# Optimization experiments

Measured on AMD Instinct MI355X. Metric: run time of the kernel, lower is better.

Reference implementation:

```python
import jax, jax.numpy as jnp
import numpy as np

N_NODES = 50000
N_EDGES = 800000
IN_FEATS = 256
H_FEATS = 256
NUM_CLASSES = 128


def setup_inputs() -> dict:
    key = jax.random.key(0)
    ks = jax.random.split(key, 5)
    x = jax.random.normal(ks[0], (N_NODES, IN_FEATS), dtype=jnp.float32)
    src = jax.random.randint(ks[1], (N_EDGES,), 0, N_NODES, dtype=jnp.int64)
    dst = jax.random.randint(ks[2], (N_EDGES,), 0, N_NODES, dtype=jnp.int64)
    W1 = jax.random.normal(ks[3], (IN_FEATS, H_FEATS), dtype=jnp.float32) * (1.0 / np.sqrt(IN_FEATS))
    b1 = jnp.zeros((H_FEATS,), dtype=jnp.float32)
    W2 = jax.random.normal(ks[4], (H_FEATS, NUM_CLASSES), dtype=jnp.float32) * (1.0 / np.sqrt(H_FEATS))
    b2 = jnp.zeros((NUM_CLASSES,), dtype=jnp.float32)
    return {"x": x, "src": src, "dst": dst, "W1": W1, "b1": b1, "W2": W2, "b2": b2}


def _graph_conv(x, src, dst, norm_src, norm_dst, W, b):
    # DGL GraphConv, norm='both': D_out^{-1/2} A D_in^{-1/2} X W + b
    # project first (in_feats >= out_feats -> cheaper messages), math identical
    h = (x * norm_src[:, None]) @ W                      # [N, out]
    agg = jax.ops.segment_sum(h[src], dst, num_segments=N_NODES)  # gather + scatter-add
    return agg * norm_dst[:, None] + b


def reference(x, src, dst, W1, b1, W2, b2):
    ones = jnp.ones((N_EDGES,), dtype=x.dtype)
    deg_out = jax.ops.segment_sum(ones, src, num_segments=N_NODES)
    deg_in = jax.ops.segment_sum(ones, dst, num_segments=N_NODES)
    norm_src = jnp.clip(deg_out, 1.0, None) ** -0.5
    norm_dst = jnp.clip(deg_in, 1.0, None) ** -0.5

    h = _graph_conv(x, src, dst, norm_src, norm_dst, W1, b1)
    h = jax.nn.relu(h)
    out = _graph_conv(h, src, dst, norm_src, norm_dst, W2, b2)
    return out
```

## Files before the change

kernel.cpp:

```cpp
#include <hip/hip_runtime.h>

#define NNODES 50000
#define MPAD   50048
#define NEDGES 800000
#define KDIM   256
#define FH     256
#define FOUT   128
#define FCH    32

#define SHIFT  8
#define NBUCK  196
#define NB1    200
#define EPB    4000

typedef __bf16 bf16x8 __attribute__((ext_vector_type(8)));
typedef float floatx4 __attribute__((ext_vector_type(4)));
typedef float floatx2 __attribute__((ext_vector_type(2)));

struct int4u { int x, y, z, w; };

__device__ __forceinline__ float bf2f(unsigned short u) {
    union { unsigned int i; float f; } v;
    v.i = ((unsigned int)u) << 16;
    return v.f;
}
__device__ __forceinline__ unsigned short f2bf(float f) {
    union { float f; unsigned int i; } v;
    v.f = f;
    unsigned int r = v.i + 0x7FFFu + ((v.i >> 16) & 1u);
    return (unsigned short)(r >> 16);
}

__device__ __forceinline__ void acc_pairs(floatx2* acc, uint4 v) {
    unsigned int d[4] = {v.x, v.y, v.z, v.w};
#pragma unroll
    for (int k = 0; k < 4; ++k) {
        union { unsigned int u; float f; } lo, hi;
        lo.u = d[k] << 16;
        hi.u = d[k] & 0xFFFF0000u;
        floatx2 p = {lo.f, hi.f};
        acc[k] += p;
    }
}

__global__ __launch_bounds__(256) void l1_sort_cast(const int* __restrict__ src,
                                                    const int* __restrict__ dst,
                                                    unsigned int* __restrict__ tmp1,
                                                    unsigned char* __restrict__ tmp2,
                                                    int* __restrict__ exD_arr,
                                                    int* __restrict__ exS_arr,
                                                    const float* __restrict__ W1,
                                                    unsigned short* __restrict__ Wt1,
                                                    const float* __restrict__ W2,
                                                    unsigned short* __restrict__ Wt2) {
    __shared__ int histD[256], histS[256], exD[256], exS[256];
    __shared__ unsigned int bufD[EPB];
    __shared__ unsigned short bufS[EPB];
    __shared__ float tile[32][33];
    const int tid = threadIdx.x;

    if (blockIdx.x >= NB1) {
        int b = blockIdx.x - NB1;
        const float* W; unsigned short* Wt; int N;
        if (b < 64) { W = W1; Wt = Wt1; N = FH; }
        else        { b -= 64; W = W2; Wt = Wt2; N = FOUT; }
        int kt = (b & 7) * 32;
        int nt = (b >> 3) * 32;
        int tx = tid & 31;
        int ty = tid >> 5;
        for (int r = ty; r < 32; r += 8)
            tile[r][tx] = W[(size_t)(kt + r) * N + nt + tx];
        __syncthreads();
        for (int r = ty; r < 32; r += 8)
            Wt[(size_t)(nt + r) * KDIM + kt + tx] = f2bf(tile[tx][r]);
        return;
    }

    const int b = blockIdx.x;
    const int base = b * EPB;
    histD[tid] = 0; histS[tid] = 0;
    __syncthreads();
    for (int g = tid; g < EPB / 4; g += 256) {
        uint4 s4 = *(const uint4*)(src + base + g * 4);
        uint4 d4 = *(const uint4*)(dst + base + g * 4);
        atomicAdd(&histD[d4.x >> SHIFT], 1);
        atomicAdd(&histD[d4.y >> SHIFT], 1);
        atomicAdd(&histD[d4.z >> SHIFT], 1);
        atomicAdd(&histD[d4.w >> SHIFT], 1);
        atomicAdd(&histS[s4.x >> SHIFT], 1);
        atomicAdd(&histS[s4.y >> SHIFT], 1);
        atomicAdd(&histS[s4.z >> SHIFT], 1);
        atomicAdd(&histS[s4.w >> SHIFT], 1);
    }
    __syncthreads();
    int vD = histD[tid], vS = histS[tid];
    exD[tid] = vD; exS[tid] = vS;
    __syncthreads();
    for (int off = 1; off < 256; off <<= 1) {
        int tD = (tid >= off) ? exD[tid - off] : 0;
        int tS = (tid >= off) ? exS[tid - off] : 0;
        __syncthreads();
        exD[tid] += tD; exS[tid] += tS;
        __syncthreads();
    }
    int eD = exD[tid] - vD, eS = exS[tid] - vS;
    exD_arr[tid * NB1 + b] = eD;
    exS_arr[tid * NB1 + b] = eS;
    __syncthreads();
    histD[tid] = eD; histS[tid] = eS;
    __syncthreads();
    for (int g = tid; g < EPB / 4; g += 256) {
        uint4 s4 = *(const uint4*)(src + base + g * 4);
        uint4 d4 = *(const uint4*)(dst + base + g * 4);
        unsigned int ss[4] = {s4.x, s4.y, s4.z, s4.w};
        unsigned int dd[4] = {d4.x, d4.y, d4.z, d4.w};
#pragma unroll
        for (int j = 0; j < 4; ++j) {
            int p = atomicAdd(&histD[dd[j] >> SHIFT], 1);
            bufD[p] = (ss[j] << 16) | dd[j];
            int q = atomicAdd(&histS[ss[j] >> SHIFT], 1);
            bufS[q] = (unsigned short)ss[j];
        }
    }
    __syncthreads();
    for (int e = tid; e < EPB; e += 256) tmp1[base + e] = bufD[e];
    for (int e = tid; e < EPB; e += 256) tmp2[base + e] = (unsigned char)(bufS[e] & 255u);
}

__global__ __launch_bounds__(256) void l2_both(const unsigned int* __restrict__ tmp1,
                                               const unsigned char* __restrict__ tmp2,
                                               const int* __restrict__ exD_arr,
                                               const int* __restrict__ exS_arr,
                                               int* __restrict__ row_ptr,
                                               float* __restrict__ norm_dst,
                                               float* __restrict__ norm_src,
                                               int* __restrict__ csr_src) {
    __shared__ int cnt[256], ofs[256], cur[256], red[256];
    __shared__ int segoff[NB1], seglen[NB1];
    const int tid = threadIdx.x;

    if (blockIdx.x >= NBUCK) {
        const int k = blockIdx.x - NBUCK;
        if (tid < NB1) {
            int e0 = exS_arr[k * NB1 + tid];
            segoff[tid] = tid * EPB + e0;
            seglen[tid] = exS_arr[(k + 1) * NB1 + tid] - e0;
        }
        cnt[tid] = 0;
        __syncthreads();
        if (tid < NB1) {
            int so = segoff[tid], sl = seglen[tid];
            for (int i = 0; i < sl; ++i)
                atomicAdd(&cnt[tmp2[so + i]], 1);
        }
        __syncthreads();
        int node = k * 256 + tid;
        if (node < NNODES) {
            int d = cnt[tid] < 1 ? 1 : cnt[tid];
            norm_src[node] = 1.0f / sqrtf((float)d);
        }
        return;
    }

    const int k = blockIdx.x;
    int e0v = 0;
    if (tid < NB1) {
        e0v = exD_arr[k * NB1 + tid];
        segoff[tid] = tid * EPB + e0v;
        seglen[tid] = exD_arr[(k + 1) * NB1 + tid] - e0v;
    }
    red[tid] = (tid < NB1) ? e0v : 0;
    cnt[tid] = 0;
    __syncthreads();
    for (int off = 128; off > 0; off >>= 1) {
        if (tid < off) red[tid] += red[tid + off];
        __syncthreads();
    }
    const int base = red[0];
    if (tid < NB1) {
        int so = segoff[tid], sl = seglen[tid];
        for (int i = 0; i < sl; ++i)
            atomicAdd(&cnt[tmp1[so + i] & 255u], 1);
    }
    __syncthreads();
    int v = cnt[tid];
    ofs[tid] = v;
    __syncthreads();
    for (int off = 1; off < 256; off <<= 1) {
        int t = (tid >= off) ? ofs[tid - off] : 0;
        __syncthreads();
        ofs[tid] += t;
        __syncthreads();
    }
    int excl = ofs[tid] - v;
    int node = k * 256 + tid;
    if (node < NNODES) {
        row_ptr[node] = base + excl;
        int d = v < 1 ? 1 : v;
        norm_dst[node] = 1.0f / sqrtf((float)d);
    }
    cur[tid] = base + excl;
    if (k == 0 && tid == 0) row_ptr[NNODES] = NEDGES;
    __syncthreads();
    if (tid < NB1) {
        int so = segoff[tid], sl = seglen[tid];
        for (int i = 0; i < sl; ++i) {
            unsigned int p = tmp1[so + i];
            int pos = atomicAdd(&cur[p & 255u], 1);
            csr_src[pos] = (int)(p >> 16);
        }
    }
}

struct arawF { float4 v[8]; float sc; };
struct arawU { uint4 v[4]; };
template <typename TA> struct rawsel;
template <> struct rawsel<float> { using type = arawF; };
template <> struct rawsel<unsigned short> { using type = arawU; };

__device__ __forceinline__ void loadA_raw(const float* A, const float* norm,
                                          int mt, int arow, int akseg, arawF& r) {
    int row = mt * 64 + arow;
    if (row < NNODES) {
        const float* p = A + (size_t)row * KDIM + akseg;
#pragma unroll
        for (int j = 0; j < 8; ++j) r.v[j] = *(const float4*)(p + j * 4);
        r.sc = norm[row];
    } else {
        float4 z = {0.f, 0.f, 0.f, 0.f};
#pragma unroll
        for (int j = 0; j < 8; ++j) r.v[j] = z;
        r.sc = 0.f;
    }
}
__device__ __forceinline__ void loadA_raw(const unsigned short* A, const float*,
                                          int mt, int arow, int akseg, arawU& r) {
    const unsigned short* p = A + ((size_t)(akseg >> 5) * MPAD + mt * 64 + arow) * FCH;
#pragma unroll
    for (int j = 0; j < 4; ++j) r.v[j] = *(const uint4*)(p + j * 8);
}
__device__ __forceinline__ void writeA_lds(char* Asb, int arow, int akseg, const arawF& r) {
    const int s = (arow & 7) << 4;
    const int base = arow * 512;
#pragma unroll
    for (int j = 0; j < 4; ++j) {
        union { uint4 u; unsigned short h[8]; } o;
        float4 a = r.v[2 * j], b = r.v[2 * j + 1];
        o.h[0] = f2bf(a.x * r.sc); o.h[1] = f2bf(a.y * r.sc);
        o.h[2] = f2bf(a.z * r.sc); o.h[3] = f2bf(a.w * r.sc);
        o.h[4] = f2bf(b.x * r.sc); o.h[5] = f2bf(b.y * r.sc);
        o.h[6] = f2bf(b.z * r.sc); o.h[7] = f2bf(b.w * r.sc);
        *(uint4*)(Asb + base + (((akseg + j * 8) * 2) ^ s)) = o.u;
    }
}
__device__ __forceinline__ void writeA_lds(char* Asb, int arow, int akseg, const arawU& r) {
    const int s = (arow & 7) << 4;
    const int base = arow * 512;
#pragma unroll
    for (int j = 0; j < 4; ++j)
        *(uint4*)(Asb + base + (((akseg + j * 8) * 2) ^ s)) = r.v[j];
}

template <typename TA, bool SCALE, int NPANEL>
__global__ __launch_bounds__(512) void gemm_bres(const TA* __restrict__ A,
                                                 const unsigned short* __restrict__ Bt,
                                                 const float* __restrict__ norm,
                                                 unsigned short* __restrict__ C) {
    constexpr int NTILES = MPAD / 64;
    __shared__ __align__(16) unsigned short Bs[128 * 256];
    __shared__ __align__(16) unsigned short As[64 * 256];
    char* Bsb = (char*)Bs;
    char* Asb = (char*)As;

    const int tid = threadIdx.x;
    const int lane = tid & 63;
    const int wave = tid >> 6;

    int col0, mt0, mstep;
    if (NPANEL == 2) {
        col0 = ((blockIdx.x >> 3) & 1) * 128;
        mt0 = ((blockIdx.x >> 4) << 3) + (blockIdx.x & 7);
        mstep = gridDim.x >> 1;
    } else {
        col0 = 0;
        mt0 = blockIdx.x;
        mstep = gridDim.x;
    }

    {
        int col = tid >> 2;
        int kq = (tid & 3) * 64;
        const unsigned short* bg = Bt + (size_t)(col0 + col) * KDIM + kq;
        const int s = (col & 7) << 4;
        const int base = col * 512;
#pragma unroll
        for (int j = 0; j < 8; ++j) {
            uint4 v = *(const uint4*)(bg + j * 8);
            *(uint4*)(Bsb + base + (((kq + j * 8) * 2) ^ s)) = v;
        }
    }

    const int arow = tid >> 3;
    const int akseg = (tid & 7) * 32;

    typename rawsel<TA>::type buf;
    loadA_raw(A, norm, mt0, arow, akseg, buf);
    writeA_lds(Asb, arow, akseg, buf);
    __syncthreads();
    int mt = mt0, mtn = mt0 + mstep;
    if (mtn < NTILES) loadA_raw(A, norm, mtn, arow, akseg, buf);

    const int wn = wave & 3, wm = wave >> 2;
    const int ar = lane & 15;
    const int fkb = (lane >> 4) << 4;
    const int rA0 = wm * 32 + ar,  rA1 = rA0 + 16;
    const int cB0 = wn * 32 + ar,  cB1 = cB0 + 16;
    const int aO0 = rA0 * 512, aS0 = (rA0 & 7) << 4;
    const int aO1 = rA1 * 512, aS1 = (rA1 & 7) << 4;
    const int bO0 = cB0 * 512, bS0 = (cB0 & 7) << 4;
    const int bO1 = cB1 * 512, bS1 = (cB1 & 7) << 4;
    const int rb = (lane >> 4) << 2, cc = lane & 15;

    unsigned short* Cb = C + ((size_t)((col0 >> 5) + wn) * MPAD) * FCH;

    for (;;) {
        floatx4 a00 = {}, a01 = {}, a10 = {}, a11 = {};
#pragma unroll
        for (int kk = 0; kk < 8; ++kk) {
            const int kb = kk * 64 + fkb;
            bf16x8 fa0 = *(const bf16x8*)(Asb + aO0 + (kb ^ aS0));
            bf16x8 fa1 = *(const bf16x8*)(Asb + aO1 + (kb ^ aS1));
            bf16x8 fb0 = *(const bf16x8*)(Bsb + bO0 + (kb ^ bS0));
            bf16x8 fb1 = *(const bf16x8*)(Bsb + bO1 + (kb ^ bS1));
            a00 = __builtin_amdgcn_mfma_f32_16x16x32_bf16(fa0, fb0, a00, 0, 0, 0);
            a01 = __builtin_amdgcn_mfma_f32_16x16x32_bf16(fa0, fb1, a01, 0, 0, 0);
            a10 = __builtin_amdgcn_mfma_f32_16x16x32_bf16(fa1, fb0, a10, 0, 0, 0);
            a11 = __builtin_amdgcn_mfma_f32_16x16x32_bf16(fa1, fb1, a11, 0, 0, 0);
        }
        {
            const int mBase = mt * 64 + wm * 32 + rb;
#pragma unroll
            for (int r = 0; r < 4; ++r) {
                int m = mBase + r;
                Cb[(size_t)m * FCH + cc]      = f2bf(a00[r]);
                Cb[(size_t)m * FCH + cc + 16] = f2bf(a01[r]);
                int m2 = m + 16;
                Cb[(size_t)m2 * FCH + cc]      = f2bf(a10[r]);
                Cb[(size_t)m2 * FCH + cc + 16] = f2bf(a11[r]);
            }
        }
        if (mtn >= NTILES) break;
        __syncthreads();
        writeA_lds(Asb, arow, akseg, buf);
        mt = mtn; mtn += mstep;
        __syncthreads();
        if (mtn < NTILES) loadA_raw(A, norm, mtn, arow, akseg, buf);
    }
}

__global__ __launch_bounds__(256) void agg1_kernel(const unsigned short* __restrict__ H,
                                                   const int* __restrict__ row_ptr,
                                                   const int* __restrict__ csr_src,
                                                   const float* __restrict__ norm_dst,
                                                   const float* __restrict__ norm_src,
                                                   const float* __restrict__ bias,
                                                   unsigned short* __restrict__ out) {
    const int c = blockIdx.x & 7;
    const int nb = blockIdx.x >> 3;
    const int tid = threadIdx.x;
    const int lane = tid & 63;
    const int g = lane >> 2;
    const int f0 = (lane & 3) * 8;
    const int node = nb * 64 + (tid >> 6) * 16 + g;

    const unsigned short* Hc = H + ((size_t)c * MPAD) * FCH + f0;
    floatx2 acc[4] = {};

    int e0 = 0, e1 = 0;
    if (node < NNODES) { e0 = row_ptr[node]; e1 = row_ptr[node + 1]; }

    if (e0 < e1) {
        int4u ia = *(const int4u*)(csr_src + e0);
        int4u ib = *(const int4u*)(csr_src + e0 + 4);
        for (int e = e0; e < e1; e += 8) {
            const int ecnt = e1 - e;
            int idx[8] = {ia.x, ia.y, ia.z, ia.w, ib.x, ib.y, ib.z, ib.w};
#pragma unroll
            for (int j = 1; j < 8; ++j) idx[j] = (j < ecnt) ? idx[j] : NNODES;
            if (e + 8 < e1) {
                ia = *(const int4u*)(csr_src + e + 8);
                ib = *(const int4u*)(csr_src + e + 12);
            }
            uint4 w[8];
#pragma unroll
            for (int j = 0; j < 8; ++j)
                w[j] = *(const uint4*)(Hc + (size_t)idx[j] * FCH);
#pragma unroll
            for (int j = 0; j < 8; ++j) acc_pairs(acc, w[j]);
        }
    }

    float nd = 0.f, ns = 0.f;
    if (node < NNODES) { nd = norm_dst[node]; ns = norm_src[node]; }
    const int fg = c * FCH + f0;
    float4 b0 = *(const float4*)(bias + fg);
    float4 b1v = *(const float4*)(bias + fg + 4);
    float bb[8] = {b0.x, b0.y, b0.z, b0.w, b1v.x, b1v.y, b1v.z, b1v.w};
    union { uint4 u; unsigned short s[8]; } o;
#pragma unroll
    for (int k = 0; k < 4; ++k) {
        o.s[2 * k]     = f2bf(fmaxf(fmaf(acc[k].x, nd, bb[2 * k]), 0.f) * ns);
        o.s[2 * k + 1] = f2bf(fmaxf(fmaf(acc[k].y, nd, bb[2 * k + 1]), 0.f) * ns);
    }
    *(uint4*)(out + ((size_t)c * MPAD + node) * FCH + f0) = o.u;
}

__global__ __launch_bounds__(256) void agg2_kernel(const unsigned short* __restrict__ H,
                                                   const int* __restrict__ row_ptr,
                                                   const int* __restrict__ csr_src,
                                                   const float* __restrict__ norm_dst,
                                                   const float* __restrict__ bias,
                                                   float* __restrict__ out) {
    const int c = (blockIdx.x & 7) >> 1;
    const int nb = (blockIdx.x >> 3) * 2 + (blockIdx.x & 1);
    const int tid = threadIdx.x;
    const int lane = tid & 63;
    const int g = lane >> 2;
    const int f0 = (lane & 3) * 8;
    const int node = nb * 64 + (tid >> 6) * 16 + g;
    if (node >= NNODES) return;

    const unsigned short* Hc = H + ((size_t)c * MPAD) * FCH + f0;
    floatx2 acc[4] = {};

    int e0 = row_ptr[node];
    int e1 = row_ptr[node + 1];

    if (e0 < e1) {
        int4u ia = *(const int4u*)(csr_src + e0);
        int4u ib = *(const int4u*)(csr_src + e0 + 4);
        for (int e = e0; e < e1; e += 8) {
            const int ecnt = e1 - e;
            int idx[8] = {ia.x, ia.y, ia.z, ia.w, ib.x, ib.y, ib.z, ib.w};
#pragma unroll
            for (int j = 1; j < 8; ++j) idx[j] = (j < ecnt) ? idx[j] : NNODES;
            if (e + 8 < e1) {
                ia = *(const int4u*)(csr_src + e + 8);
                ib = *(const int4u*)(csr_src + e + 12);
            }
            uint4 w[8];
#pragma unroll
            for (int j = 0; j < 8; ++j)
                w[j] = *(const uint4*)(Hc + (size_t)idx[j] * FCH);
#pragma unroll
            for (int j = 0; j < 8; ++j) acc_pairs(acc, w[j]);
        }
    }

    float nd = norm_dst[node];
    const int fg = c * FCH + f0;
    float4 b0 = *(const float4*)(bias + fg);
    float4 b1v = *(const float4*)(bias + fg + 4);
    float4 o1, o2;
    o1.x = fmaf(acc[0].x, nd, b0.x);
    o1.y = fmaf(acc[0].y, nd, b0.y);
    o1.z = fmaf(acc[1].x, nd, b0.z);
    o1.w = fmaf(acc[1].y, nd, b0.w);
    o2.x = fmaf(acc[2].x, nd, b1v.x);
    o2.y = fmaf(acc[2].y, nd, b1v.y);
    o2.z = fmaf(acc[3].x, nd, b1v.z);
    o2.w = fmaf(acc[3].y, nd, b1v.w);
    *(float4*)(out + (size_t)node * FOUT + fg) = o1;
    *(float4*)(out + (size_t)node * FOUT + fg + 4) = o2;
}

extern "C" void kernel_launch(void* const* d_in, const int* in_sizes, int n_in,
                              void* d_out, int out_size, void* d_ws, size_t ws_size,
                              hipStream_t stream) {
    const float* x   = (const float*)d_in[0];
    const int*   src = (const int*)d_in[1];
    const int*   dst = (const int*)d_in[2];
    const float* W1  = (const float*)d_in[3];
    const float* b1  = (const float*)d_in[4];
    const float* W2  = (const float*)d_in[5];
    const float* b2  = (const float*)d_in[6];
    float* out = (float*)d_out;

    char* ws = (char*)d_ws;
    size_t off = 0;
    auto alloc = [&](size_t bytes) {
        char* p = ws + off;
        off += (bytes + 255) & ~(size_t)255;
        return p;
    };
    float* norm_src  = (float*)alloc(NNODES * 4);
    float* norm_dst  = (float*)alloc(NNODES * 4);
    int*   exD_arr   = (int*)alloc((size_t)256 * NB1 * 4);
    int*   exS_arr   = (int*)alloc((size_t)256 * NB1 * 4);
    unsigned int*  tmp1 = (unsigned int*)alloc((size_t)NEDGES * 4);
    unsigned char* tmp2 = (unsigned char*)alloc((size_t)NEDGES);
    int*   row_ptr   = (int*)alloc((NNODES + 16) * 4);
    int*   csr_src   = (int*)alloc((size_t)(NEDGES + 256) * 4);
    unsigned short* h   = (unsigned short*)alloc((size_t)MPAD * FH * 2);
    unsigned short* h1  = (unsigned short*)alloc((size_t)MPAD * FH * 2);
    unsigned short* Wt1 = (unsigned short*)alloc((size_t)FH * KDIM * 2);
    unsigned short* Wt2 = (unsigned short*)alloc((size_t)FOUT * KDIM * 2);
    unsigned short* h2  = h;

    l1_sort_cast<<<NB1 + 96, 256, 0, stream>>>(src, dst, tmp1, tmp2, exD_arr, exS_arr,
                                               W1, Wt1, W2, Wt2);
    l2_both<<<2 * NBUCK, 256, 0, stream>>>(tmp1, tmp2, exD_arr, exS_arr,
                                           row_ptr, norm_dst, norm_src, csr_src);

    gemm_bres<float, true, 2><<<512, 512, 0, stream>>>(x, Wt1, norm_src, h);
    agg1_kernel<<<(MPAD / 64) * 8, 256, 0, stream>>>(h, row_ptr, csr_src, norm_dst, norm_src, b1, h1);

    gemm_bres<unsigned short, false, 1><<<256, 512, 0, stream>>>(h1, Wt2, nullptr, h2);
    agg2_kernel<<<((MPAD / 64 + 1) / 2) * 8, 256, 0, stream>>>(h2, row_ptr, csr_src, norm_dst, b2, out);
}
```

Before: 239.1 us.

## Pad CSR rows to multiples of eight and degree-sort nodes for aggregation

Each destination node's edge list is padded to a multiple of 8 with a sentinel index, in fixed per-bucket regions, and its offset and iteration count are packed into one word. This removes the per-iteration tail masking and the row_ptr pair load. An extra block in the first GEMM launch builds a permutation of nodes sorted by iteration count, so the aggregation kernels process nodes of similar degree together and reduce wave divergence. In exchange it adds an indirection load per node, scatters the output writes, gathers extra sentinel rows, and runs a single-block serial counting sort inside the GEMM.

```diff
diff --git a/kernel.cpp b/kernel.cpp
--- a/kernel.cpp
+++ b/kernel.cpp
@@ -12,12 +12,11 @@
 #define NBUCK  196
 #define NB1    200
 #define EPB    4000
+#define EPBK   8192
 
 typedef __bf16 bf16x8 __attribute__((ext_vector_type(8)));
 typedef float floatx4 __attribute__((ext_vector_type(4)));
 typedef float floatx2 __attribute__((ext_vector_type(2)));
-
-struct int4u { int x, y, z, w; };
 
 __device__ __forceinline__ float bf2f(unsigned short u) {
     union { unsigned int i; float f; } v;
@@ -131,12 +130,13 @@
                                                const unsigned char* __restrict__ tmp2,
                                                const int* __restrict__ exD_arr,
                                                const int* __restrict__ exS_arr,
-                                               int* __restrict__ row_ptr,
+                                               unsigned int* __restrict__ rp8,
                                                float* __restrict__ norm_dst,
                                                float* __restrict__ norm_src,
-                                               int* __restrict__ csr_src) {
-    __shared__ int cnt[256], ofs[256], cur[256], red[256];
+                                               int* __restrict__ csr8) {
+    __shared__ int cnt[256], ofs[256], cur[256];
     __shared__ int segoff[NB1], seglen[NB1];
+    __shared__ int ptot;
     const int tid = threadIdx.x;
 
     if (blockIdx.x >= NBUCK) {
@@ -163,20 +163,13 @@
     }
 
     const int k = blockIdx.x;
-    int e0v = 0;
     if (tid < NB1) {
-        e0v = exD_arr[k * NB1 + tid];
-        segoff[tid] = tid * EPB + e0v;
-        seglen[tid] = exD_arr[(k + 1) * NB1 + tid] - e0v;
-    }
-    red[tid] = (tid < NB1) ? e0v : 0;
+        int e0 = exD_arr[k * NB1 + tid];
+        segoff[tid] = tid * EPB + e0;
+        seglen[tid] = exD_arr[(k + 1) * NB1 + tid] - e0;
+    }
     cnt[tid] = 0;
     __syncthreads();
-    for (int off = 128; off > 0; off >>= 1) {
-        if (tid < off) red[tid] += red[tid + off];
-        __syncthreads();
-    }
-    const int base = red[0];
     if (tid < NB1) {
         int so = segoff[tid], sl = seglen[tid];
         for (int i = 0; i < sl; ++i)
@@ -184,7 +177,8 @@
     }
     __syncthreads();
     int v = cnt[tid];
-    ofs[tid] = v;
+    int p8 = ((v + 7) >> 3) << 3;
+    ofs[tid] = p8;
     __syncthreads();
     for (int off = 1; off < 256; off <<= 1) {
         int t = (tid >= off) ? ofs[tid - off] : 0;
@@ -192,22 +186,25 @@
         ofs[tid] += t;
         __syncthreads();
     }
-    int excl = ofs[tid] - v;
+    int innerStart = ofs[tid] - p8;
+    if (tid == 255) ptot = ofs[255];
+    __syncthreads();
+    const int kb = k * EPBK;
+    for (int i = tid; i < ptot; i += 256) csr8[kb + i] = NNODES;
     int node = k * 256 + tid;
     if (node < NNODES) {
-        row_ptr[node] = base + excl;
+        rp8[node] = ((unsigned int)(kb + innerStart) << 6) | (unsigned int)((v + 7) >> 3);
         int d = v < 1 ? 1 : v;
         norm_dst[node] = 1.0f / sqrtf((float)d);
     }
-    cur[tid] = base + excl;
-    if (k == 0 && tid == 0) row_ptr[NNODES] = NEDGES;
+    cur[tid] = kb + innerStart;
     __syncthreads();
     if (tid < NB1) {
         int so = segoff[tid], sl = seglen[tid];
         for (int i = 0; i < sl; ++i) {
             unsigned int p = tmp1[so + i];
             int pos = atomicAdd(&cur[p & 255u], 1);
-            csr_src[pos] = (int)(p >> 16);
+            csr8[pos] = (int)(p >> 16);
         }
     }
 }
@@ -261,11 +258,13 @@
         *(uint4*)(Asb + base + (((akseg + j * 8) * 2) ^ s)) = r.v[j];
 }
 
-template <typename TA, bool SCALE, int NPANEL>
+template <typename TA, bool SCALE, int NPANEL, int EXTRA>
 __global__ __launch_bounds__(512) void gemm_bres(const TA* __restrict__ A,
                                                  const unsigned short* __restrict__ Bt,
                                                  const float* __restrict__ norm,
-                                                 unsigned short* __restrict__ C) {
+                                                 unsigned short* __restrict__ C,
+                                                 const unsigned int* __restrict__ rp8,
+                                                 int* __restrict__ perm) {
     constexpr int NTILES = MPAD / 64;
     __shared__ __align__(16) unsigned short Bs[128 * 256];
     __shared__ __align__(16) unsigned short As[64 * 256];
@@ -273,6 +272,30 @@
     char* Asb = (char*)As;
 
     const int tid = threadIdx.x;
+    const int ngrid = (int)gridDim.x - EXTRA;
+
+    if constexpr (EXTRA > 0) {
+        if ((int)blockIdx.x >= ngrid) {
+            __shared__ int hist[64], curs[64];
+            for (int i = tid; i < 64; i += 512) hist[i] = 0;
+            __syncthreads();
+            for (int n = tid; n < NNODES; n += 512)
+                atomicAdd(&hist[rp8[n] & 63u], 1);
+            __syncthreads();
+            if (tid == 0) {
+                int s = 0;
+                for (int i = 0; i < 64; ++i) { curs[i] = s; s += hist[i]; }
+            }
+            __syncthreads();
+            for (int n = tid; n < NNODES; n += 512) {
+                int c = rp8[n] & 63u;
+                int pos = atomicAdd(&curs[c], 1);
+                perm[pos] = n;
+            }
+            return;
+        }
+    }
+
     const int lane = tid & 63;
     const int wave = tid >> 6;
 
@@ -280,11 +303,11 @@
     if (NPANEL == 2) {
         col0 = ((blockIdx.x >> 3) & 1) * 128;
         mt0 = ((blockIdx.x >> 4) << 3) + (blockIdx.x & 7);
-        mstep = gridDim.x >> 1;
+        mstep = ngrid >> 1;
     } else {
         col0 = 0;
         mt0 = blockIdx.x;
-        mstep = gridDim.x;
+        mstep = ngrid;
     }
 
     {
@@ -359,8 +382,9 @@
 }
 
 __global__ __launch_bounds__(256) void agg1_kernel(const unsigned short* __restrict__ H,
-                                                   const int* __restrict__ row_ptr,
-                                                   const int* __restrict__ csr_src,
+                                                   const unsigned int* __restrict__ rp8,
+                                                   const int* __restrict__ csr8,
+                                                   const int* __restrict__ perm,
                                                    const float* __restrict__ norm_dst,
                                                    const float* __restrict__ norm_src,
                                                    const float* __restrict__ bias,
@@ -371,25 +395,24 @@
     const int lane = tid & 63;
     const int g = lane >> 2;
     const int f0 = (lane & 3) * 8;
-    const int node = nb * 64 + (tid >> 6) * 16 + g;
+    const int slot = nb * 64 + (tid >> 6) * 16 + g;
+    const int node = (slot < NNODES) ? perm[slot] : slot;
 
     const unsigned short* Hc = H + ((size_t)c * MPAD) * FCH + f0;
     floatx2 acc[4] = {};
 
-    int e0 = 0, e1 = 0;
-    if (node < NNODES) { e0 = row_ptr[node]; e1 = row_ptr[node + 1]; }
-
-    if (e0 < e1) {
-        int4u ia = *(const int4u*)(csr_src + e0);
-        int4u ib = *(const int4u*)(csr_src + e0 + 4);
-        for (int e = e0; e < e1; e += 8) {
-            const int ecnt = e1 - e;
+    unsigned int packed = (node < NNODES) ? rp8[node] : 0u;
+    int niter = (int)(packed & 63u);
+    const int* cp = csr8 + (packed >> 6);
+
+    if (niter > 0) {
+        int4 ia = *(const int4*)cp;
+        int4 ib = *(const int4*)(cp + 4);
+        for (int it = 0; it < niter; ++it) {
             int idx[8] = {ia.x, ia.y, ia.z, ia.w, ib.x, ib.y, ib.z, ib.w};
-#pragma unroll
-            for (int j = 1; j < 8; ++j) idx[j] = (j < ecnt) ? idx[j] : NNODES;
-            if (e + 8 < e1) {
-                ia = *(const int4u*)(csr_src + e + 8);
-                ib = *(const int4u*)(csr_src + e + 12);
+            if (it + 1 < niter) {
+                ia = *(const int4*)(cp + (it + 1) * 8);
+                ib = *(const int4*)(cp + (it + 1) * 8 + 4);
             }
             uint4 w[8];
 #pragma unroll
@@ -416,8 +439,9 @@
 }
 
 __global__ __launch_bounds__(256) void agg2_kernel(const unsigned short* __restrict__ H,
-                                                   const int* __restrict__ row_ptr,
-                                                   const int* __restrict__ csr_src,
+                                                   const unsigned int* __restrict__ rp8,
+                                                   const int* __restrict__ csr8,
+                                                   const int* __restrict__ perm,
                                                    const float* __restrict__ norm_dst,
                                                    const float* __restrict__ bias,
                                                    float* __restrict__ out) {
@@ -427,26 +451,25 @@
     const int lane = tid & 63;
     const int g = lane >> 2;
     const int f0 = (lane & 3) * 8;
-    const int node = nb * 64 + (tid >> 6) * 16 + g;
-    if (node >= NNODES) return;
+    const int slot = nb * 64 + (tid >> 6) * 16 + g;
+    if (slot >= NNODES) return;
+    const int node = perm[slot];
 
     const unsigned short* Hc = H + ((size_t)c * MPAD) * FCH + f0;
     floatx2 acc[4] = {};
 
-    int e0 = row_ptr[node];
-    int e1 = row_ptr[node + 1];
-
-    if (e0 < e1) {
-        int4u ia = *(const int4u*)(csr_src + e0);
-        int4u ib = *(const int4u*)(csr_src + e0 + 4);
-        for (int e = e0; e < e1; e += 8) {
-            const int ecnt = e1 - e;
+    unsigned int packed = rp8[node];
+    int niter = (int)(packed & 63u);
+    const int* cp = csr8 + (packed >> 6);
+
+    if (niter > 0) {
+        int4 ia = *(const int4*)cp;
+        int4 ib = *(const int4*)(cp + 4);
+        for (int it = 0; it < niter; ++it) {
             int idx[8] = {ia.x, ia.y, ia.z, ia.w, ib.x, ib.y, ib.z, ib.w};
-#pragma unroll
-            for (int j = 1; j < 8; ++j) idx[j] = (j < ecnt) ? idx[j] : NNODES;
-            if (e + 8 < e1) {
-                ia = *(const int4u*)(csr_src + e + 8);
-                ib = *(const int4u*)(csr_src + e + 12);
+            if (it + 1 < niter) {
+                ia = *(const int4*)(cp + (it + 1) * 8);
+                ib = *(const int4*)(cp + (it + 1) * 8 + 4);
             }
             uint4 w[8];
 #pragma unroll
@@ -499,8 +522,9 @@
     int*   exS_arr   = (int*)alloc((size_t)256 * NB1 * 4);
     unsigned int*  tmp1 = (unsigned int*)alloc((size_t)NEDGES * 4);
     unsigned char* tmp2 = (unsigned char*)alloc((size_t)NEDGES);
-    int*   row_ptr   = (int*)alloc((NNODES + 16) * 4);
-    int*   csr_src   = (int*)alloc((size_t)(NEDGES + 256) * 4);
+    unsigned int* rp8 = (unsigned int*)alloc((size_t)NNODES * 4);
+    int*   csr8      = (int*)alloc((size_t)NBUCK * EPBK * 4);
+    int*   perm      = (int*)alloc((size_t)NNODES * 4);
     unsigned short* h   = (unsigned short*)alloc((size_t)MPAD * FH * 2);
     unsigned short* h1  = (unsigned short*)alloc((size_t)MPAD * FH * 2);
     unsigned short* Wt1 = (unsigned short*)alloc((size_t)FH * KDIM * 2);
@@ -510,11 +534,14 @@
     l1_sort_cast<<<NB1 + 96, 256, 0, stream>>>(src, dst, tmp1, tmp2, exD_arr, exS_arr,
                                                W1, Wt1, W2, Wt2);
     l2_both<<<2 * NBUCK, 256, 0, stream>>>(tmp1, tmp2, exD_arr, exS_arr,
-                                           row_ptr, norm_dst, norm_src, csr_src);
-
-    gemm_bres<float, true, 2><<<512, 512, 0, stream>>>(x, Wt1, norm_src, h);
-    agg1_kernel<<<(MPAD / 64) * 8, 256, 0, stream>>>(h, row_ptr, csr_src, norm_dst, norm_src, b1, h1);
-
-    gemm_bres<unsigned short, false, 1><<<256, 512, 0, stream>>>(h1, Wt2, nullptr, h2);
-    agg2_kernel<<<((MPAD / 64 + 1) / 2) * 8, 256, 0, stream>>>(h2, row_ptr, csr_src, norm_dst, b2, out);
-}
+                                           rp8, norm_dst, norm_src, csr8);
+
+    gemm_bres<float, true, 2, 1><<<513, 512, 0, stream>>>(x, Wt1, norm_src, h, rp8, perm);
+    agg1_kernel<<<(MPAD / 64) * 8, 256, 0, stream>>>(h, rp8, csr8, perm,
+                                                     norm_dst, norm_src, b1, h1);
+
+    gemm_bres<unsigned short, false, 1, 0><<<256, 512, 0, stream>>>(h1, Wt2, nullptr, h2,
+                                                                    rp8, nullptr);
+    agg2_kernel<<<((MPAD / 64 + 1) / 2) * 8, 256, 0, stream>>>(h2, rp8, csr8, perm,
+                                                               norm_dst, b2, out);
+}
```

Result: slower. 299.6 us (+25.3%).

## Load GEMM A fragments directly from global memory, drop A LDS staging

Applied to the files above, without the earlier changes.

The GEMM no longer stages A tiles through shared memory with a register prefetch and two barriers per tile. Each wave now loads its MFMA A fragments straight from global memory, scaling and converting to bf16 in registers. The B columns are permuted in LDS so adjacent output columns can be packed into 32-bit stores, and the second GEMM's grid is doubled to 512 blocks. This removes LDS traffic and barriers and raises occupancy, at the cost of less coalesced global reads and no explicit prefetch overlap.

```diff
diff --git a/kernel.cpp b/kernel.cpp
--- a/kernel.cpp
+++ b/kernel.cpp
@@ -212,53 +212,19 @@
     }
 }
 
-struct arawF { float4 v[8]; float sc; };
-struct arawU { uint4 v[4]; };
-template <typename TA> struct rawsel;
-template <> struct rawsel<float> { using type = arawF; };
-template <> struct rawsel<unsigned short> { using type = arawU; };
-
-__device__ __forceinline__ void loadA_raw(const float* A, const float* norm,
-                                          int mt, int arow, int akseg, arawF& r) {
-    int row = mt * 64 + arow;
-    if (row < NNODES) {
-        const float* p = A + (size_t)row * KDIM + akseg;
-#pragma unroll
-        for (int j = 0; j < 8; ++j) r.v[j] = *(const float4*)(p + j * 4);
-        r.sc = norm[row];
-    } else {
-        float4 z = {0.f, 0.f, 0.f, 0.f};
-#pragma unroll
-        for (int j = 0; j < 8; ++j) r.v[j] = z;
-        r.sc = 0.f;
-    }
-}
-__device__ __forceinline__ void loadA_raw(const unsigned short* A, const float*,
-                                          int mt, int arow, int akseg, arawU& r) {
-    const unsigned short* p = A + ((size_t)(akseg >> 5) * MPAD + mt * 64 + arow) * FCH;
-#pragma unroll
-    for (int j = 0; j < 4; ++j) r.v[j] = *(const uint4*)(p + j * 8);
-}
-__device__ __forceinline__ void writeA_lds(char* Asb, int arow, int akseg, const arawF& r) {
-    const int s = (arow & 7) << 4;
-    const int base = arow * 512;
-#pragma unroll
-    for (int j = 0; j < 4; ++j) {
-        union { uint4 u; unsigned short h[8]; } o;
-        float4 a = r.v[2 * j], b = r.v[2 * j + 1];
-        o.h[0] = f2bf(a.x * r.sc); o.h[1] = f2bf(a.y * r.sc);
-        o.h[2] = f2bf(a.z * r.sc); o.h[3] = f2bf(a.w * r.sc);
-        o.h[4] = f2bf(b.x * r.sc); o.h[5] = f2bf(b.y * r.sc);
-        o.h[6] = f2bf(b.z * r.sc); o.h[7] = f2bf(b.w * r.sc);
-        *(uint4*)(Asb + base + (((akseg + j * 8) * 2) ^ s)) = o.u;
-    }
-}
-__device__ __forceinline__ void writeA_lds(char* Asb, int arow, int akseg, const arawU& r) {
-    const int s = (arow & 7) << 4;
-    const int base = arow * 512;
-#pragma unroll
-    for (int j = 0; j < 4; ++j)
-        *(uint4*)(Asb + base + (((akseg + j * 8) * 2) ^ s)) = r.v[j];
+__device__ __forceinline__ bf16x8 a_frag(const unsigned short* A, int row, int kk, int fe, float) {
+    return *(const bf16x8*)(A + ((size_t)kk * MPAD + row) * FCH + fe);
+}
+__device__ __forceinline__ bf16x8 a_frag(const float* A, int row, int kk, int fe, float sc) {
+    const float* p = A + (size_t)row * KDIM + kk * 32 + fe;
+    float4 v0 = *(const float4*)p;
+    float4 v1 = *(const float4*)(p + 4);
+    union { bf16x8 b; unsigned short s[8]; } r;
+    r.s[0] = f2bf(v0.x * sc); r.s[1] = f2bf(v0.y * sc);
+    r.s[2] = f2bf(v0.z * sc); r.s[3] = f2bf(v0.w * sc);
+    r.s[4] = f2bf(v1.x * sc); r.s[5] = f2bf(v1.y * sc);
+    r.s[6] = f2bf(v1.z * sc); r.s[7] = f2bf(v1.w * sc);
+    return r.b;
 }
 
 template <typename TA, bool SCALE, int NPANEL>
@@ -268,9 +234,7 @@
                                                  unsigned short* __restrict__ C) {
     constexpr int NTILES = MPAD / 64;
     __shared__ __align__(16) unsigned short Bs[128 * 256];
-    __shared__ __align__(16) unsigned short As[64 * 256];
     char* Bsb = (char*)Bs;
-    char* Asb = (char*)As;
 
     const int tid = threadIdx.x;
     const int lane = tid & 63;
@@ -291,70 +255,58 @@
         int col = tid >> 2;
         int kq = (tid & 3) * 64;
         const unsigned short* bg = Bt + (size_t)(col0 + col) * KDIM + kq;
-        const int s = (col & 7) << 4;
-        const int base = col * 512;
+        int w = col & 31;
+        int slot = (col & ~31) + ((w & 1) << 4) + (w >> 1);
+        const int s = (slot & 7) << 4;
+        const int sbase = slot * 512;
 #pragma unroll
         for (int j = 0; j < 8; ++j) {
             uint4 v = *(const uint4*)(bg + j * 8);
-            *(uint4*)(Bsb + base + (((kq + j * 8) * 2) ^ s)) = v;
-        }
-    }
-
-    const int arow = tid >> 3;
-    const int akseg = (tid & 7) * 32;
-
-    typename rawsel<TA>::type buf;
-    loadA_raw(A, norm, mt0, arow, akseg, buf);
-    writeA_lds(Asb, arow, akseg, buf);
-    __syncthreads();
-    int mt = mt0, mtn = mt0 + mstep;
-    if (mtn < NTILES) loadA_raw(A, norm, mtn, arow, akseg, buf);
+            *(uint4*)(Bsb + sbase + (((kq + j * 8) * 2) ^ s)) = v;
+        }
+    }
+    __syncthreads();
 
     const int wn = wave & 3, wm = wave >> 2;
     const int ar = lane & 15;
-    const int fkb = (lane >> 4) << 4;
-    const int rA0 = wm * 32 + ar,  rA1 = rA0 + 16;
-    const int cB0 = wn * 32 + ar,  cB1 = cB0 + 16;
-    const int aO0 = rA0 * 512, aS0 = (rA0 & 7) << 4;
-    const int aO1 = rA1 * 512, aS1 = (rA1 & 7) << 4;
+    const int fe = (lane >> 4) << 3;
+    const int fkb = fe * 2;
+    const int cB0 = wn * 32 + ar, cB1 = cB0 + 16;
     const int bO0 = cB0 * 512, bS0 = (cB0 & 7) << 4;
     const int bO1 = cB1 * 512, bS1 = (cB1 & 7) << 4;
     const int rb = (lane >> 4) << 2, cc = lane & 15;
-
     unsigned short* Cb = C + ((size_t)((col0 >> 5) + wn) * MPAD) * FCH;
 
-    for (;;) {
+    for (int mt = mt0; mt < NTILES; mt += mstep) {
+        const int r0 = mt * 64 + wm * 32 + ar;
+        const int r1 = r0 + 16;
+        int ra0 = r0, ra1 = r1;
+        float sc0 = 1.f, sc1 = 1.f;
+        if (SCALE) {
+            ra0 = (r0 < NNODES) ? r0 : 0; sc0 = (r0 < NNODES) ? norm[r0] : 0.f;
+            ra1 = (r1 < NNODES) ? r1 : 0; sc1 = (r1 < NNODES) ? norm[r1] : 0.f;
+        }
+
         floatx4 a00 = {}, a01 = {}, a10 = {}, a11 = {};
 #pragma unroll
         for (int kk = 0; kk < 8; ++kk) {
-            const int kb = kk * 64 + fkb;
-            bf16x8 fa0 = *(const bf16x8*)(Asb + aO0 + (kb ^ aS0));
-            bf16x8 fa1 = *(const bf16x8*)(Asb + aO1 + (kb ^ aS1));
-            bf16x8 fb0 = *(const bf16x8*)(Bsb + bO0 + (kb ^ bS0));
-            bf16x8 fb1 = *(const bf16x8*)(Bsb + bO1 + (kb ^ bS1));
+            bf16x8 fa0 = a_frag(A, ra0, kk, fe, sc0);
+            bf16x8 fa1 = a_frag(A, ra1, kk, fe, sc1);
+            bf16x8 fb0 = *(const bf16x8*)(Bsb + bO0 + ((kk * 64 + fkb) ^ bS0));
+            bf16x8 fb1 = *(const bf16x8*)(Bsb + bO1 + ((kk * 64 + fkb) ^ bS1));
             a00 = __builtin_amdgcn_mfma_f32_16x16x32_bf16(fa0, fb0, a00, 0, 0, 0);
             a01 = __builtin_amdgcn_mfma_f32_16x16x32_bf16(fa0, fb1, a01, 0, 0, 0);
             a10 = __builtin_amdgcn_mfma_f32_16x16x32_bf16(fa1, fb0, a10, 0, 0, 0);
             a11 = __builtin_amdgcn_mfma_f32_16x16x32_bf16(fa1, fb1, a11, 0, 0, 0);
         }
-        {
-            const int mBase = mt * 64 + wm * 32 + rb;
-#pragma unroll
-            for (int r = 0; r < 4; ++r) {
-                int m = mBase + r;
-                Cb[(size_t)m * FCH + cc]      = f2bf(a00[r]);
-                Cb[(size_t)m * FCH + cc + 16] = f2bf(a01[r]);
-                int m2 = m + 16;
-                Cb[(size_t)m2 * FCH + cc]      = f2bf(a10[r]);
-                Cb[(size_t)m2 * FCH + cc + 16] = f2bf(a11[r]);
-            }
-        }
-        if (mtn >= NTILES) break;
-        __syncthreads();
-        writeA_lds(Asb, arow, akseg, buf);
-        mt = mtn; mtn += mstep;
-        __syncthreads();
-        if (mtn < NTILES) loadA_raw(A, norm, mtn, arow, akseg, buf);
+        const int mB = mt * 64 + wm * 32 + rb;
+#pragma unroll
+        for (int r = 0; r < 4; ++r) {
+            unsigned int u0 = (unsigned int)f2bf(a00[r]) | ((unsigned int)f2bf(a01[r]) << 16);
+            unsigned int u1 = (unsigned int)f2bf(a10[r]) | ((unsigned int)f2bf(a11[r]) << 16);
+            *(unsigned int*)(Cb + (size_t)(mB + r) * FCH + 2 * cc) = u0;
+            *(unsigned int*)(Cb + (size_t)(mB + r + 16) * FCH + 2 * cc) = u1;
+        }
     }
 }
 
@@ -513,8 +465,10 @@
                                            row_ptr, norm_dst, norm_src, csr_src);
 
     gemm_bres<float, true, 2><<<512, 512, 0, stream>>>(x, Wt1, norm_src, h);
-    agg1_kernel<<<(MPAD / 64) * 8, 256, 0, stream>>>(h, row_ptr, csr_src, norm_dst, norm_src, b1, h1);
-
-    gemm_bres<unsigned short, false, 1><<<256, 512, 0, stream>>>(h1, Wt2, nullptr, h2);
-    agg2_kernel<<<((MPAD / 64 + 1) / 2) * 8, 256, 0, stream>>>(h2, row_ptr, csr_src, norm_dst, b2, out);
-}
+    agg1_kernel<<<(MPAD / 64) * 8, 256, 0, stream>>>(h, row_ptr, csr_src,
+                                                     norm_dst, norm_src, b1, h1);
+
+    gemm_bres<unsigned short, false, 1><<<512, 512, 0, stream>>>(h1, Wt2, nullptr, h2);
+    agg2_kernel<<<((MPAD / 64 + 1) / 2) * 8, 256, 0, stream>>>(h2, row_ptr, csr_src,
+                                                               norm_dst, b2, out);
+}
```

Result: slower. 250.3 us (+4.7%).
